# Kernel tuning notes

Measured on AMD Instinct MI355X. Metric: run time of the kernel, lower is better.

## Reference

```python
import jax, jax.numpy as jnp
import numpy as np

# Workspace layout (static slice bounds, per init_kwargs)
SS, SE = 0, 512        # spoke
HPS, HPE = 512, 768    # hub private
HSS, HSE = 768, 1024   # hub shared
TS, TE = 1024, 1088    # tag
HS, HE = 512, 1024     # full hub (priv + shared) for the read path

B, T, D_STATE, D_MODEL, D_LATENT = 8, 4096, 1088, 1024, 128


def setup_inputs() -> dict:
    key = jax.random.key(0)
    ks = jax.random.split(key, 10)
    scale = 0.02  # typical init scale for learned projections
    return {
        "S": jax.random.normal(ks[0], (B, T, D_STATE), jnp.float32),
        "w_spoke": jax.random.normal(ks[1], (B, T, SE - SS), jnp.float32),
        "w_hub_priv": jax.random.normal(ks[2], (B, T, HPE - HPS), jnp.float32),
        "w_hub_shared": jax.random.normal(ks[3], (B, T, HSE - HSS), jnp.float32),
        "tag": jax.random.normal(ks[4], (B, T, TE - TS), jnp.float32),
        "W_read": jax.random.normal(ks[5], (D_MODEL, D_STATE), jnp.float32) * scale,
        "cache": jnp.zeros((B, T, D_LATENT), jnp.float32),
        "latent": jax.random.normal(ks[6], (B, T, D_LATENT), jnp.float32),
        "Wk": jax.random.normal(ks[7], (D_MODEL, D_LATENT), jnp.float32) * scale,
        "Wv": jax.random.normal(ks[8], (D_MODEL, D_LATENT), jnp.float32) * scale,
    }


def reference(S, w_spoke, w_hub_priv, w_hub_shared, tag, W_read, cache, latent, Wk, Wv):
    # --- fused_workspace_write: four independent slice-adds into S ---
    S = S.at[:, :, SS:SE].add(w_spoke)
    S = S.at[:, :, HPS:HPE].add(w_hub_priv)
    S = S.at[:, :, HSS:HSE].add(w_hub_shared)
    S = S.at[:, :, TS:TE].add(tag)

    # --- fused_workspace_read: concat(spoke, hub, tag) then F.linear(., W_read) ---
    readable = jnp.concatenate(
        [S[:, :, SS:SE], S[:, :, HS:HE], S[:, :, TS:TE]], axis=-1
    )  # (B, T, D_STATE)
    out = jnp.einsum("btr,dr->btd", readable, W_read)  # (B, T, D_MODEL)

    # --- CWTLatentCache.update: overwrite latents at start_position=0 ---
    cache = jax.lax.dynamic_update_slice(cache, latent, (0, 0, 0))

    # --- K/V reconstruction from compressed latents via up-projections ---
    k = jnp.einsum("btl,dl->btd", cache, Wk)  # (B, T, D_MODEL)
    v = jnp.einsum("btl,dl->btd", cache, Wv)  # (B, T, D_MODEL)
    return (out, k, v)
```

## Files before the change

kernel.cpp:

```cpp
#include <hip/hip_runtime.h>

typedef __attribute__((ext_vector_type(8))) _Float16 half8;
typedef __attribute__((ext_vector_type(2))) __fp16 half2r;
typedef __attribute__((ext_vector_type(4))) float f32x4;

#define AS1 __attribute__((address_space(1)))
#define AS3 __attribute__((address_space(3)))

union H2U { half2r h; unsigned int u; };
union Frag { half8 v; unsigned long long d[2]; };

__device__ __forceinline__ unsigned int pk(float a, float b) {
    H2U x; x.h = __builtin_amdgcn_cvt_pkrtz(a, b); return x.u;
}

__device__ __forceinline__ void gload_lds16(const void* g, void* l) {
    __builtin_amdgcn_global_load_lds((const AS1 unsigned int*)g,
                                     (AS3 unsigned int*)l, 16, 0, 0);
}

#define W1_ROWB 2176
#define WS2_OFF 2228224
#define W2_ROWB 256
#define A_ROWB  2176

__device__ __forceinline__ void pick_w(int ks, const float* wsp, const float* whp,
                                       const float* whs, const float* wtg,
                                       const float*& wbase, int& wstr, int& wko) {
    if (ks < 8)       { wbase = wsp; wstr = 512; wko = ks * 64; }
    else if (ks < 12) { wbase = whp; wstr = 256; wko = ks * 64 - 512; }
    else if (ks < 16) { wbase = whs; wstr = 256; wko = ks * 64 - 768; }
    else              { wbase = wtg; wstr = 64;  wko = 0; }
}

__global__ __launch_bounds__(256) void prep_w(const float* __restrict__ Wr,
                                              const float* __restrict__ Wk,
                                              const float* __restrict__ Wv,
                                              char* __restrict__ ws) {
    int id = blockIdx.x * 256 + threadIdx.x;
    if (id < 272 * 1024) {
        int n = id / 272;
        int k = (id % 272) * 4;
        f32x4 w = *(const f32x4*)(Wr + (size_t)n * 1088 + k);
        uint2 q; q.x = pk(w.x, w.y); q.y = pk(w.z, w.w);
        size_t off = (size_t)n * W1_ROWB + ((k >> 5) << 6)
                   + ((((k >> 2) & 7) ^ (n & 7)) << 3);
        *(uint2*)(ws + off) = q;
    } else {
        int j = id - 272 * 1024;
        int r = j >> 5;
        int k = (j & 31) << 2;
        const float* src = (r < 1024) ? (Wk + (size_t)r * 128 + k)
                                      : (Wv + (size_t)(r - 1024) * 128 + k);
        f32x4 w = *(const f32x4*)src;
        uint2 q; q.x = pk(w.x, w.y); q.y = pk(w.z, w.w);
        size_t off = WS2_OFF + (size_t)r * W2_ROWB + ((k >> 6) << 7)
                   + (((k & 63) << 1) ^ ((r & 7) << 4));
        *(uint2*)(ws + off) = q;
    }
}

__global__ __launch_bounds__(256)
void fuse_a(const float* __restrict__ S, const float* __restrict__ wsp,
            const float* __restrict__ whp, const float* __restrict__ whs,
            const float* __restrict__ wtg, char* __restrict__ a16) {
    int u = blockIdx.x * 256 + threadIdx.x;
    int row = u / 272;
    int rem = u % 272;
    int ks = rem >> 4;
    int k4 = (rem & 15) << 2;

    const float* wbase; int wstr, wko;
    pick_w(ks, wsp, whp, whs, wtg, wbase, wstr, wko);

    f32x4 s4 = *(const f32x4*)(S + (size_t)row * 1088 + ks * 64 + k4);
    f32x4 w4 = *(const f32x4*)(wbase + (size_t)row * wstr + wko + k4);
    uint2 q; q.x = pk(s4.x + w4.x, s4.y + w4.y);
             q.y = pk(s4.z + w4.z, s4.w + w4.w);
    int kk = ks * 64 + k4;
    size_t off = (size_t)row * A_ROWB + ((kk >> 5) << 6)
               + ((((kk >> 2) & 7) ^ (row & 7)) << 3);
    *(uint2*)(a16 + off) = q;
}

__global__ __launch_bounds__(256, 4)
void gemm_read(const char* __restrict__ wsA, const char* __restrict__ wws,
               float* __restrict__ out) {
    __shared__ char lds[32768];

    int bid = blockIdx.x;
    int wg   = (bid & 7) * 256 + (bid >> 3);
    int mblk = wg >> 3, nblk = wg & 7;
    int m0 = mblk << 7, n0 = nblk << 7;

    int tid = threadIdx.x;
    int lane = tid & 63, wid = tid >> 6;
    int wm = (wid >> 1) << 6, wn = (wid & 1) << 6;
    int lp = lane & 15, lg = lane >> 4;

    f32x4 acc[4][4] = {};

#define STAGE32(T, DL, BASE, ROWB, R0) do {                               \
        const char* grow = (BASE) + (size_t)(R0) * (ROWB) + (T) * 64;     \
        _Pragma("unroll")                                                 \
        for (int c = 0; c < 2; ++c) {                                     \
            int s = c * 4096 + wid * 1024 + lane * 16;                    \
            int rr = s >> 6, cb = s & 63;                                 \
            gload_lds16(grow + (size_t)rr * (ROWB) + cb,                  \
                        (DL) + c * 4096 + wid * 1024);                    \
        }                                                                 \
    } while (0)

#define COMPUTE32(AL, BL) do {                                            \
        Frag af[4], bf[4];                                                \
        _Pragma("unroll")                                                 \
        for (int f = 0; f < 4; ++f) {                                     \
            int ra = wm + f * 16 + lp;  int xa = ra & 7;                  \
            af[f].d[0] = *(const unsigned long long*)((AL) + (ra << 6) + ((lg ^ xa) << 3));        \
            af[f].d[1] = *(const unsigned long long*)((AL) + (ra << 6) + (((4 + lg) ^ xa) << 3));  \
            int rb = wn + f * 16 + lp;  int xb = rb & 7;                  \
            bf[f].d[0] = *(const unsigned long long*)((BL) + (rb << 6) + ((lg ^ xb) << 3));        \
            bf[f].d[1] = *(const unsigned long long*)((BL) + (rb << 6) + (((4 + lg) ^ xb) << 3));  \
        }                                                                 \
        _Pragma("unroll")                                                 \
        for (int i = 0; i < 4; ++i)                                       \
            _Pragma("unroll")                                             \
            for (int j = 0; j < 4; ++j)                                   \
                acc[i][j] = __builtin_amdgcn_mfma_f32_16x16x32_f16(af[i].v, bf[j].v, acc[i][j], 0, 0, 0); \
    } while (0)

    STAGE32(0, lds,         wsA, A_ROWB,  m0);
    STAGE32(0, lds + 16384, wws, W1_ROWB, n0);
    __syncthreads();

    for (int t = 0; t < 34; ++t) {
        int co = (t & 1) ? 8192 : 0;
        int no = co ^ 8192;
        if (t < 33) {
            STAGE32(t + 1, lds + no,         wsA, A_ROWB,  m0);
            STAGE32(t + 1, lds + 16384 + no, wws, W1_ROWB, n0);
        }
        COMPUTE32(lds + co, lds + 16384 + co);
        __syncthreads();
    }

    #pragma unroll
    for (int i = 0; i < 4; ++i)
        #pragma unroll
        for (int j = 0; j < 4; ++j) {
            int row = m0 + wm + i * 16 + (lg << 2);
            int col = n0 + wn + j * 16 + lp;
            float* p = out + (size_t)row * 1024 + col;
            #pragma unroll
            for (int r = 0; r < 4; ++r) p[(size_t)r * 1024] = acc[i][j][r];
        }
#undef STAGE32
#undef COMPUTE32
}

__global__ __launch_bounds__(256, 2)
void gemm_kv(const float* __restrict__ lat, const char* __restrict__ ws2,
             float* __restrict__ outk, float* __restrict__ outv) {
    __shared__ char lds[32768];
    char* Al = lds;
    char* Bl = lds + 16384;

    int bid = blockIdx.x;
    int wg   = (bid & 7) * 512 + (bid >> 3);
    int mblk = wg >> 4, nb = wg & 15;
    int m0 = mblk << 7;
    int nrow0 = nb << 7;
    float* out = (nb < 8) ? outk : outv;
    int n0 = (nb & 7) << 7;

    int tid = threadIdx.x;
    int lane = tid & 63, wid = tid >> 6;
    int wm = (wid >> 1) << 6, wn = (wid & 1) << 6;
    int lp = lane & 15, lg = lane >> 4;

    f32x4 acc[4][4] = {};

    for (int ks = 0; ks < 2; ++ks) {
        __syncthreads();
        {
            const char* wrow = ws2 + (size_t)nrow0 * W2_ROWB + ks * 128;
            #pragma unroll
            for (int c = 0; c < 4; ++c) {
                int s = c * 4096 + wid * 1024 + lane * 16;
                int n = s >> 7, cb = s & 127;
                gload_lds16(wrow + (size_t)n * W2_ROWB + cb,
                            Bl + c * 4096 + wid * 1024);
            }
        }
        #pragma unroll
        for (int i = 0; i < 8; ++i) {
            int u = i * 256 + tid;
            int row = u >> 4;
            int k4 = (u & 15) << 2;
            f32x4 s4 = *(const f32x4*)(lat + (size_t)(m0 + row) * 128 + ks * 64 + k4);
            uint2 q; q.x = pk(s4.x, s4.y); q.y = pk(s4.z, s4.w);
            *(uint2*)(Al + (row << 7) + ((k4 << 1) ^ ((row & 7) << 4))) = q;
        }
        __syncthreads();

        #pragma unroll
        for (int b = 0; b < 2; ++b) {
            Frag af[4], bf[4];
            #pragma unroll
            for (int f = 0; f < 4; ++f) {
                int ra = wm + f * 16 + lp;  int xa = (ra & 7) << 4;
                af[f].d[0] = *(const unsigned long long*)(Al + (ra << 7) + ((b * 64 + lg * 8) ^ xa));
                af[f].d[1] = *(const unsigned long long*)(Al + (ra << 7) + ((b * 64 + 32 + lg * 8) ^ xa));
                int rb = wn + f * 16 + lp;  int xb = (rb & 7) << 4;
                bf[f].d[0] = *(const unsigned long long*)(Bl + (rb << 7) + ((b * 64 + lg * 8) ^ xb));
                bf[f].d[1] = *(const unsigned long long*)(Bl + (rb << 7) + ((b * 64 + 32 + lg * 8) ^ xb));
            }
            #pragma unroll
            for (int i = 0; i < 4; ++i)
                #pragma unroll
                for (int j = 0; j < 4; ++j)
                    acc[i][j] = __builtin_amdgcn_mfma_f32_16x16x32_f16(af[i].v, bf[j].v, acc[i][j], 0, 0, 0);
        }
    }

    #pragma unroll
    for (int i = 0; i < 4; ++i)
        #pragma unroll
        for (int j = 0; j < 4; ++j) {
            int row = m0 + wm + i * 16 + (lg << 2);
            int col = n0 + wn + j * 16 + lp;
            float* p = out + (size_t)row * 1024 + col;
            #pragma unroll
            for (int r = 0; r < 4; ++r) p[(size_t)r * 1024] = acc[i][j][r];
        }
}

extern "C" void kernel_launch(void* const* d_in, const int* in_sizes, int n_in,
                              void* d_out, int out_size, void* d_ws, size_t ws_size,
                              hipStream_t stream) {
    const float* S   = (const float*)d_in[0];
    const float* wsp = (const float*)d_in[1];
    const float* whp = (const float*)d_in[2];
    const float* whs = (const float*)d_in[3];
    const float* wtg = (const float*)d_in[4];
    const float* Wr  = (const float*)d_in[5];
    const float* lat = (const float*)d_in[7];
    const float* Wk  = (const float*)d_in[8];
    const float* Wv  = (const float*)d_in[9];
    float* out = (float*)d_out;
    char*  ws  = (char*)d_ws;

    char* a16 = (char*)(out + 67108864ull);

    hipLaunchKernelGGL(prep_w, dim3(1344), dim3(256), 0, stream, Wr, Wk, Wv, ws);
    hipLaunchKernelGGL(fuse_a, dim3(34816), dim3(256), 0, stream,
                       S, wsp, whp, whs, wtg, a16);
    hipLaunchKernelGGL(gemm_read, dim3(2048), dim3(256), 0, stream,
                       a16, ws, out);
    hipLaunchKernelGGL(gemm_kv, dim3(4096), dim3(256), 0, stream,
                       lat, ws + WS2_OFF, out + 33554432ull, out + 67108864ull);
}
```

Baseline: 270.7 us.

## Keep full-K weight slab resident in LDS and stream A directly from global

The read GEMM is restructured so each 512-thread block loads a 64-column slice of the full-K f16 weight (about 136 KB) into LDS once. Each wave then computes 128 rows by reading A fragments straight from global memory, with no staging or double buffering. This removes the per-K-step barriers and repeated weight staging, and the A buffer is written in plain row-major order. In exchange, LDS use per block is much larger, A reuse across the N tiles now depends on caches, and the global loads for A are uncoalesced 8-byte per-lane reads with no explicit latency hiding.

```diff
diff --git a/kernel.cpp b/kernel.cpp
--- a/kernel.cpp
+++ b/kernel.cpp
@@ -19,10 +19,9 @@
                                      (AS3 unsigned int*)l, 16, 0, 0);
 }
 
-#define W1_ROWB 2176
+#define ROWB    2176
 #define WS2_OFF 2228224
 #define W2_ROWB 256
-#define A_ROWB  2176
 
 __device__ __forceinline__ void pick_w(int ks, const float* wsp, const float* whp,
                                        const float* whs, const float* wtg,
@@ -43,8 +42,9 @@
         int k = (id % 272) * 4;
         f32x4 w = *(const f32x4*)(Wr + (size_t)n * 1088 + k);
         uint2 q; q.x = pk(w.x, w.y); q.y = pk(w.z, w.w);
-        size_t off = (size_t)n * W1_ROWB + ((k >> 5) << 6)
-                   + ((((k >> 2) & 7) ^ (n & 7)) << 3);
+        int l = k * 2;
+        size_t off = (size_t)n * ROWB + (l & ~127)
+                   + ((l & 127) ^ ((n & 7) << 4));
         *(uint2*)(ws + off) = q;
     } else {
         int j = id - 272 * 1024;
@@ -77,85 +77,73 @@
     f32x4 w4 = *(const f32x4*)(wbase + (size_t)row * wstr + wko + k4);
     uint2 q; q.x = pk(s4.x + w4.x, s4.y + w4.y);
              q.y = pk(s4.z + w4.z, s4.w + w4.w);
-    int kk = ks * 64 + k4;
-    size_t off = (size_t)row * A_ROWB + ((kk >> 5) << 6)
-               + ((((kk >> 2) & 7) ^ (row & 7)) << 3);
-    *(uint2*)(a16 + off) = q;
-}
-
-__global__ __launch_bounds__(256, 4)
-void gemm_read(const char* __restrict__ wsA, const char* __restrict__ wws,
+    *(uint2*)(a16 + (size_t)row * ROWB + (size_t)(ks * 64 + k4) * 2) = q;
+}
+
+__global__ __launch_bounds__(512, 2)
+void gemm_read(const char* __restrict__ a16, const char* __restrict__ wws,
                float* __restrict__ out) {
-    __shared__ char lds[32768];
+    __shared__ char Bl[139264];
 
     int bid = blockIdx.x;
-    int wg   = (bid & 7) * 256 + (bid >> 3);
-    int mblk = wg >> 3, nblk = wg & 7;
-    int m0 = mblk << 7, n0 = nblk << 7;
+    int wg   = (bid & 7) * 64 + (bid >> 3);
+    int mg = wg >> 4, nb = wg & 15;
+    int n0 = nb << 6;
 
     int tid = threadIdx.x;
     int lane = tid & 63, wid = tid >> 6;
-    int wm = (wid >> 1) << 6, wn = (wid & 1) << 6;
     int lp = lane & 15, lg = lane >> 4;
-
-    f32x4 acc[4][4] = {};
-
-#define STAGE32(T, DL, BASE, ROWB, R0) do {                               \
-        const char* grow = (BASE) + (size_t)(R0) * (ROWB) + (T) * 64;     \
-        _Pragma("unroll")                                                 \
-        for (int c = 0; c < 2; ++c) {                                     \
-            int s = c * 4096 + wid * 1024 + lane * 16;                    \
-            int rr = s >> 6, cb = s & 63;                                 \
-            gload_lds16(grow + (size_t)rr * (ROWB) + cb,                  \
-                        (DL) + c * 4096 + wid * 1024);                    \
-        }                                                                 \
-    } while (0)
-
-#define COMPUTE32(AL, BL) do {                                            \
-        Frag af[4], bf[4];                                                \
-        _Pragma("unroll")                                                 \
-        for (int f = 0; f < 4; ++f) {                                     \
-            int ra = wm + f * 16 + lp;  int xa = ra & 7;                  \
-            af[f].d[0] = *(const unsigned long long*)((AL) + (ra << 6) + ((lg ^ xa) << 3));        \
-            af[f].d[1] = *(const unsigned long long*)((AL) + (ra << 6) + (((4 + lg) ^ xa) << 3));  \
-            int rb = wn + f * 16 + lp;  int xb = rb & 7;                  \
-            bf[f].d[0] = *(const unsigned long long*)((BL) + (rb << 6) + ((lg ^ xb) << 3));        \
-            bf[f].d[1] = *(const unsigned long long*)((BL) + (rb << 6) + (((4 + lg) ^ xb) << 3));  \
-        }                                                                 \
-        _Pragma("unroll")                                                 \
-        for (int i = 0; i < 4; ++i)                                       \
-            _Pragma("unroll")                                             \
-            for (int j = 0; j < 4; ++j)                                   \
-                acc[i][j] = __builtin_amdgcn_mfma_f32_16x16x32_f16(af[i].v, bf[j].v, acc[i][j], 0, 0, 0); \
-    } while (0)
-
-    STAGE32(0, lds,         wsA, A_ROWB,  m0);
-    STAGE32(0, lds + 16384, wws, W1_ROWB, n0);
+    int row0 = (mg << 10) + (wid << 7);
+
+    {
+        const char* gb = wws + (size_t)n0 * ROWB;
+        #pragma unroll
+        for (int c = 0; c < 17; ++c) {
+            int s = c * 8192 + tid * 16;
+            gload_lds16(gb + s, Bl + s);
+        }
+    }
+    asm volatile("s_waitcnt vmcnt(0)" ::: "memory");
     __syncthreads();
 
-    for (int t = 0; t < 34; ++t) {
-        int co = (t & 1) ? 8192 : 0;
-        int no = co ^ 8192;
-        if (t < 33) {
-            STAGE32(t + 1, lds + no,         wsA, A_ROWB,  m0);
-            STAGE32(t + 1, lds + 16384 + no, wws, W1_ROWB, n0);
-        }
-        COMPUTE32(lds + co, lds + 16384 + co);
-        __syncthreads();
+    f32x4 acc[8][4] = {};
+    const char* arow = a16 + (size_t)row0 * ROWB + lg * 8;
+
+    #pragma unroll 2
+    for (int h = 0; h < 34; ++h) {
+        Frag af[8], bf[4];
+        #pragma unroll
+        for (int f = 0; f < 8; ++f) {
+            const char* p = arow + (size_t)(f * 16 + lp) * ROWB + h * 64;
+            af[f].d[0] = *(const unsigned long long*)(p);
+            af[f].d[1] = *(const unsigned long long*)(p + 32);
+        }
+        #pragma unroll
+        for (int f = 0; f < 4; ++f) {
+            int rb = f * 16 + lp;
+            int x  = (rb & 7) << 4;
+            int l0 = h * 64 + lg * 8;
+            int l1 = l0 + 32;
+            bf[f].d[0] = *(const unsigned long long*)(Bl + rb * ROWB + (l0 & ~127) + ((l0 & 127) ^ x));
+            bf[f].d[1] = *(const unsigned long long*)(Bl + rb * ROWB + (l1 & ~127) + ((l1 & 127) ^ x));
+        }
+        #pragma unroll
+        for (int i = 0; i < 8; ++i)
+            #pragma unroll
+            for (int j = 0; j < 4; ++j)
+                acc[i][j] = __builtin_amdgcn_mfma_f32_16x16x32_f16(af[i].v, bf[j].v, acc[i][j], 0, 0, 0);
     }
 
     #pragma unroll
-    for (int i = 0; i < 4; ++i)
+    for (int i = 0; i < 8; ++i)
         #pragma unroll
         for (int j = 0; j < 4; ++j) {
-            int row = m0 + wm + i * 16 + (lg << 2);
-            int col = n0 + wn + j * 16 + lp;
+            int row = row0 + i * 16 + (lg << 2);
+            int col = n0 + j * 16 + lp;
             float* p = out + (size_t)row * 1024 + col;
             #pragma unroll
             for (int r = 0; r < 4; ++r) p[(size_t)r * 1024] = acc[i][j][r];
         }
-#undef STAGE32
-#undef COMPUTE32
 }
 
 __global__ __launch_bounds__(256, 2)
@@ -255,7 +243,7 @@
     hipLaunchKernelGGL(prep_w, dim3(1344), dim3(256), 0, stream, Wr, Wk, Wv, ws);
     hipLaunchKernelGGL(fuse_a, dim3(34816), dim3(256), 0, stream,
                        S, wsp, whp, whs, wtg, a16);
-    hipLaunchKernelGGL(gemm_read, dim3(2048), dim3(256), 0, stream,
+    hipLaunchKernelGGL(gemm_read, dim3(512), dim3(512), 0, stream,
                        a16, ws, out);
     hipLaunchKernelGGL(gemm_kv, dim3(4096), dim3(256), 0, stream,
                        lat, ws + WS2_OFF, out + 33554432ull, out + 67108864ull);
```

Result: slower. 431.2 us (+59.3%).
